# Optimization experiments

Measured on AMD Instinct MI355X. Metric: run time of the kernel, lower is better.

The kernel has to match this reference:

```python
import jax, jax.numpy as jnp
import numpy as np
import math

HIDDEN = 2048
NUM_HEADS = 16
NUM_KV_HEADS = 4
HEAD_DIM = 128
GROUPS = NUM_HEADS // NUM_KV_HEADS
BATCH = 1
SEQ = 4096
THETA = 10000.0


def _rope(x):
    # x: [B, h, S, D], interleaved-pair rotation as in the torch module
    seq = x.shape[2]
    freqs = 1.0 / (THETA ** (jnp.arange(0, HEAD_DIM, 2, dtype=jnp.float32) / HEAD_DIM))  # [D/2]
    angles = jnp.arange(seq, dtype=jnp.float32)[:, None] * freqs[None, :]  # [S, D/2]
    cos = jnp.cos(angles)[None, None]  # [1,1,S,D/2]
    sin = jnp.sin(angles)[None, None]
    x1 = x[..., 0::2]
    x2 = x[..., 1::2]
    # stack along new last axis then flatten -> interleaved layout
    rot = jnp.stack([x1 * cos - x2 * sin, x1 * sin + x2 * cos], axis=-1)
    return rot.reshape(x.shape)


def setup_inputs() -> dict:
    key = jax.random.key(0)
    kx, kq, kk, kv, ko = jax.random.split(key, 5)
    scale = 0.02
    x = jax.random.normal(kx, (BATCH, SEQ, HIDDEN), dtype=jnp.float32)
    Wq = jax.random.normal(kq, (NUM_HEADS * HEAD_DIM, HIDDEN), dtype=jnp.float32) * scale
    Wk = jax.random.normal(kk, (NUM_KV_HEADS * HEAD_DIM, HIDDEN), dtype=jnp.float32) * scale
    Wv = jax.random.normal(kv, (NUM_KV_HEADS * HEAD_DIM, HIDDEN), dtype=jnp.float32) * scale
    Wo = jax.random.normal(ko, (HIDDEN, NUM_HEADS * HEAD_DIM), dtype=jnp.float32) * scale
    return {"x": x, "Wq": Wq, "Wk": Wk, "Wv": Wv, "Wo": Wo}


def reference(x, Wq, Wk, Wv, Wo):
    B, S, _ = x.shape
    q = (x @ Wq.T).reshape(B, S, NUM_HEADS, HEAD_DIM).transpose(0, 2, 1, 3)      # [B,16,S,D]
    k = (x @ Wk.T).reshape(B, S, NUM_KV_HEADS, HEAD_DIM).transpose(0, 2, 1, 3)   # [B,4,S,D]
    v = (x @ Wv.T).reshape(B, S, NUM_KV_HEADS, HEAD_DIM).transpose(0, 2, 1, 3)
    q = _rope(q)
    k = _rope(k)
    # GQA: repeat_interleave KV heads across the group dim
    k = jnp.repeat(k, GROUPS, axis=1)  # [B,16,S,D]
    v = jnp.repeat(v, GROUPS, axis=1)
    scale = 1.0 / math.sqrt(HEAD_DIM)
    scores = jnp.einsum("bhqd,bhkd->bhqk", q, k) * scale  # [B,16,S,S]
    causal = jnp.triu(jnp.ones((S, S), dtype=bool), k=1)
    scores = jnp.where(causal[None, None], jnp.float32(-jnp.inf), scores)
    attn = jax.nn.softmax(scores, axis=-1)
    out = jnp.einsum("bhqk,bhkd->bhqd", attn, v)           # [B,16,S,D]
    out = out.transpose(0, 2, 1, 3).reshape(B, S, NUM_HEADS * HEAD_DIM)
    return out @ Wo.T
```

## Files before the change

### kernel.cpp

```cpp
#include <hip/hip_runtime.h>
#include <hip/hip_bf16.h>

typedef unsigned short u16;
typedef unsigned int u32;
typedef short short8 __attribute__((ext_vector_type(8)));
typedef unsigned short ushort4v __attribute__((ext_vector_type(4)));
typedef float f32x4 __attribute__((ext_vector_type(4)));
typedef float f32x16 __attribute__((ext_vector_type(16)));
typedef u32 u32x4 __attribute__((ext_vector_type(4)));

#define SEQN 4096
#define HID 2048
#define NH 16
#define NKV 4
#define HD 128
#define QDIM 2048
#define KVD 512
#define QKVS 3072

static __device__ __forceinline__ float bf2f(u16 u){
  unsigned x = ((unsigned)u) << 16; float f; __builtin_memcpy(&f, &x, 4); return f;
}
static __device__ __forceinline__ u16 f2bf(float f){
  unsigned x; __builtin_memcpy(&x, &f, 4);
  x += 0x7fffu + ((x >> 16) & 1u);
  return (u16)(x >> 16);
}
static __device__ __forceinline__ u32 pk2(float a, float b){
  return (u32)f2bf(a) | ((u32)f2bf(b) << 16);
}

__global__ __launch_bounds__(256) void cvt_kernel(const float* __restrict__ in, u16* __restrict__ out, int n4){
  int i = blockIdx.x * 256 + threadIdx.x;
  if (i >= n4) return;
  f32x4 v = ((const f32x4*)in)[i];
  ushort4v o;
  o.x = f2bf(v.x); o.y = f2bf(v.y); o.z = f2bf(v.z); o.w = f2bf(v.w);
  ((ushort4v*)out)[i] = o;
}

__global__ __launch_bounds__(256) void rope_kernel(u16* __restrict__ X, int stride, int nheads, int total){
  int idx = blockIdx.x * 256 + threadIdx.x;
  if (idx >= total) return;
  int i = idx & 63;
  int rest = idx >> 6;
  int h = rest % nheads;
  int s = rest / nheads;
  float freq = expf(-0.14391156831212788f * (float)i);
  float ang = (float)s * freq;
  float c = cosf(ang), sn = sinf(ang);
  u16* p = X + (size_t)s * stride + (size_t)h * HD + 2 * i;
  float x1 = bf2f(p[0]), x2 = bf2f(p[1]);
  p[0] = f2bf(x1 * c - x2 * sn);
  p[1] = f2bf(x1 * sn + x2 * c);
}

__global__ __launch_bounds__(256) void vtrans_kernel(const u16* __restrict__ V, int vstride, u16* __restrict__ VTg){
  __shared__ u16 T[64][72];
  const int s0 = blockIdx.x * 64;
  const int c0 = blockIdx.y * 64;
  const int tid = threadIdx.x;
  const int sl = tid & 63, ch = tid >> 6;
  const u16* src = V + (size_t)(s0 + sl) * vstride + c0 + ch * 16;
  *(short8*)&T[sl][ch * 16]     = *(const short8*)(src);
  *(short8*)&T[sl][ch * 16 + 8] = *(const short8*)(src + 8);
  __syncthreads();
#pragma unroll
  for (int it = 0; it < 16; it++){
    int c = it * 4 + ch;
    VTg[(size_t)(c0 + c) * SEQN + s0 + sl] = T[sl][c];
  }
}

static __device__ __forceinline__ void gload16(const void* g, void* l){
  __builtin_amdgcn_global_load_lds((const __attribute__((address_space(1))) void*)g,
                                   (__attribute__((address_space(3))) void*)l, 16, 0, 0);
}

template<int F32OUT>
__global__ __launch_bounds__(256) void gemm_kernel(const u16* __restrict__ A, const u16* __restrict__ B,
                                                   void* __restrict__ Cout, int M, int N, int Kd, int ldc){
  __shared__ alignas(16) u16 As[128 * 32];
  __shared__ alignas(16) u16 Bs[128 * 32];
  const int tid = threadIdx.x;
  const int w = tid >> 6, l = tid & 63;
  const int wr = w >> 1, wc = w & 1;
  const int lc = l & 15, lg = l >> 4;
  const int tm = blockIdx.x * 128, tn = blockIdx.y * 128;

  const int srow = w * 32 + (l >> 2);
  const int scol = (l & 3) * 8;
  const u16* Ag = A + (size_t)(tm + srow) * Kd + scol;
  const u16* Bg = B + (size_t)(tn + srow) * Kd + scol;
  u16* As0 = As + (w * 2) * 512;
  u16* Bs0 = Bs + (w * 2) * 512;

  f32x4 acc[4][4] = {};

  for (int k0 = 0; k0 < Kd; k0 += 32){
    gload16(Ag + k0,                    As0);
    gload16(Ag + k0 + (size_t)16 * Kd,  As0 + 512);
    gload16(Bg + k0,                    Bs0);
    gload16(Bg + k0 + (size_t)16 * Kd,  Bs0 + 512);
    __syncthreads();
    short8 a[4], b[4];
#pragma unroll
    for (int mi = 0; mi < 4; mi++) a[mi] = *(const short8*)&As[(wr*64 + mi*16 + lc) * 32 + lg*8];
#pragma unroll
    for (int ni = 0; ni < 4; ni++) b[ni] = *(const short8*)&Bs[(wc*64 + ni*16 + lc) * 32 + lg*8];
#pragma unroll
    for (int mi = 0; mi < 4; mi++)
#pragma unroll
      for (int ni = 0; ni < 4; ni++)
        acc[mi][ni] = __builtin_amdgcn_mfma_f32_16x16x32_bf16(a[mi], b[ni], acc[mi][ni], 0, 0, 0);
    __syncthreads();
  }

#pragma unroll
  for (int mi = 0; mi < 4; mi++)
#pragma unroll
    for (int ni = 0; ni < 4; ni++)
#pragma unroll
      for (int r = 0; r < 4; r++){
        int row = tm + wr*64 + mi*16 + lg*4 + r;
        int col = tn + wc*64 + ni*16 + lc;
        float v = acc[mi][ni][r];
        if (F32OUT) ((float*)Cout)[(size_t)row * ldc + col] = v;
        else        ((u16*)Cout)[(size_t)row * ldc + col] = f2bf(v);
      }
}

__global__ __launch_bounds__(256, 2) void attn_kernel(const u16* __restrict__ Qg, const u16* __restrict__ Kgb,
                                                      const u16* __restrict__ VTg, u16* __restrict__ Aout,
                                                      u16* __restrict__ PO, float* __restrict__ mP,
                                                      float* __restrict__ LP){
  __shared__ alignas(16) char pool[65536];

  const int pr  = blockIdx.x;
  const int h   = blockIdx.y;
  const int s   = blockIdx.z;
  const int kvh = h >> 2;
  const int tid = threadIdx.x;
  const int w = tid >> 6, l = tid & 63;
  const int q5 = l & 31;
  const int hi = l >> 5;
  const int hi4 = hi * 4;
  const float csc = 0.12751743f;

  const u16* Ksrc[4];
  const u16* Vsrc[4];
#pragma unroll
  for (int i = 0; i < 4; i++){
    int blk = w * 4 + i;
    int row = blk * 4 + (l >> 4);
    int cg  = (l & 15) ^ (row & 15);
    Ksrc[i] = Kgb + (size_t)row * QKVS + kvh * HD + cg * 8;
    int d   = blk * 8 + (l >> 3);
    int cv  = (l & 7) ^ (d & 7);
    Vsrc[i] = VTg + (size_t)(kvh * 128 + d) * SEQN + cv * 8;
  }

  auto issueTile = [&](int b, int kv0){
    char* Ksb = pool + b * 32768;
    char* VTb = Ksb + 16384;
#pragma unroll
    for (int i = 0; i < 4; i++)
      gload16(Ksrc[i] + (size_t)kv0 * QKVS, Ksb + (w * 4 + i) * 1024);
#pragma unroll
    for (int i = 0; i < 4; i++)
      gload16(Vsrc[i] + kv0, VTb + (w * 4 + i) * 1024);
  };

  const int qlo = pr, qhi = 31 - pr;
  int nseg, sq[2], st0[2], st1[2], smode[2];
  if (s == 0){
    nseg = 2;
    sq[0] = qlo; st0[0] = 0;           st1[0] = 2 * pr + 2;   smode[0] = 0;
    sq[1] = qhi; st0[1] = 0;           st1[1] = 31 - 2 * pr;  smode[1] = 1;
  } else {
    nseg = 1;
    sq[0] = qhi; st0[0] = 31 - 2 * pr; st1[0] = 64 - 2 * pr;  smode[0] = 2;
  }

  for (int sg = 0; sg < nseg; sg++){
    const int qt = sq[sg], t0 = st0[sg], t1 = st1[sg], mode = smode[sg];
    const int qbase = qt * 128 + w * 32;
    const int qa    = qbase + q5;

    short8 qf[8];
    {
      const u16* qp = Qg + (size_t)(qbase + q5) * QKVS + h * HD + hi * 8;
#pragma unroll
      for (int k0 = 0; k0 < 8; k0++) qf[k0] = *(const short8*)(qp + k0 * 16);
    }

    f32x16 Ov[4] = {};
    float Lrow = 0.f;
    float ms = -1e30f;

    auto computeTile = [&](int b, int kv0){
      if (kv0 > qbase + 31) return;
      char* Ksb = pool + b * 32768;
      char* VTb = Ksb + 16384;
      f32x16 Sv[2] = {};
#pragma unroll
      for (int k0 = 0; k0 < 8; k0++){
#pragma unroll
        for (int nb = 0; nb < 2; nb++){
          int kvr = nb * 32 + q5;
          short8 kf = *(const short8*)(Ksb + kvr * 256 + (((k0 * 2 + hi) ^ (kvr & 15)) << 4));
          Sv[nb] = __builtin_amdgcn_mfma_f32_32x32x16_bf16(kf, qf[k0], Sv[nb], 0, 0, 0);
        }
      }
      if (kv0 + 63 > qbase){
#pragma unroll
        for (int nb = 0; nb < 2; nb++)
#pragma unroll
          for (int r = 0; r < 16; r++){
            int kva = kv0 + nb * 32 + (r & 3) + 8 * (r >> 2) + hi4;
            if (kva > qa) Sv[nb][r] = -1e30f;
          }
      }
      float tm = -3e38f;
#pragma unroll
      for (int nb = 0; nb < 2; nb++)
#pragma unroll
        for (int r = 0; r < 16; r++) tm = fmaxf(tm, Sv[nb][r]);
      tm = fmaxf(tm, __shfl_xor(tm, 32));
      float tms = tm * csc;
      if (!__all(tms - ms <= 8.f)){
        float nms = fmaxf(ms, tms);
        float al = __builtin_amdgcn_exp2f(ms - nms);
        ms = nms;
        Lrow *= al;
#pragma unroll
        for (int nb = 0; nb < 4; nb++)
#pragma unroll
          for (int r = 0; r < 16; r++) Ov[nb][r] *= al;
      }
      float ts = 0.f;
#pragma unroll
      for (int nb = 0; nb < 2; nb++)
#pragma unroll
        for (int r = 0; r < 16; r++){
          float p = __builtin_amdgcn_exp2f(__builtin_fmaf(Sv[nb][r], csc, -ms));
          Sv[nb][r] = p;
          ts += p;
        }
      ts += __shfl_xor(ts, 32);
      Lrow += ts;
#pragma unroll
      for (int kc = 0; kc < 4; kc++){
        const int nb = kc >> 1, rb = (kc & 1) * 8;
        u32 Aw = pk2(Sv[nb][rb + 0], Sv[nb][rb + 1]);
        u32 Bw = pk2(Sv[nb][rb + 2], Sv[nb][rb + 3]);
        u32 Cw = pk2(Sv[nb][rb + 4], Sv[nb][rb + 5]);
        u32 Dw = pk2(Sv[nb][rb + 6], Sv[nb][rb + 7]);
        u32 sAw = __shfl_xor(Aw, 32);
        u32 sBw = __shfl_xor(Bw, 32);
        u32 sCw = __shfl_xor(Cw, 32);
        u32 sDw = __shfl_xor(Dw, 32);
        u32 w0 = hi ? sCw : Aw;
        u32 w1 = hi ? sDw : Bw;
        u32 w2 = hi ? Cw : sAw;
        u32 w3 = hi ? Dw : sBw;
        u32x4 pw4 = {w0, w1, w2, w3};
        short8 pf = *(short8*)&pw4;
#pragma unroll
        for (int nbd = 0; nbd < 4; nbd++){
          int drow = nbd * 32 + q5;
          short8 vf = *(const short8*)(VTb + drow * 128 + (((kc * 2 + hi) ^ (drow & 7)) << 4));
          Ov[nbd] = __builtin_amdgcn_mfma_f32_32x32x16_bf16(vf, pf, Ov[nbd], 0, 0, 0);
        }
      }
    };

    __syncthreads();
    issueTile(0, t0 * 64);
    __syncthreads();
    int cur = 0;
    for (int t = t0; t < t1; t++){
      if (t + 1 < t1) issueTile(cur ^ 1, (t + 1) * 64);
      computeTile(cur, t * 64);
      __syncthreads();
      cur ^= 1;
    }

    u16* Ew = (u16*)(pool + w * 8704);
    float rl = (mode == 0) ? (1.f / Lrow) : 1.f;
#pragma unroll
    for (int nbd = 0; nbd < 4; nbd++)
#pragma unroll
      for (int r = 0; r < 16; r += 2){
        int d = nbd * 32 + (r & 3) + 8 * (r >> 2) + hi4;
        u32 wpk = pk2(Ov[nbd][r] * rl, Ov[nbd][r + 1] * rl);
        *(u32*)((char*)Ew + q5 * 272 + d * 2) = wpk;
      }
    if (mode == 0){
#pragma unroll
      for (int pass = 0; pass < 8; pass++){
        int q2 = pass * 4 + (l >> 4);
        short8 ov = *(const short8*)((char*)Ew + q2 * 272 + (l & 15) * 16);
        *(short8*)(Aout + (size_t)(qbase + q2) * QDIM + h * HD + (l & 15) * 8) = ov;
      }
    } else {
      const int p = mode - 1;
      u16* dstb = PO + ((size_t)((p * 16 + pr) * NH + h) * 128) * 128;
#pragma unroll
      for (int pass = 0; pass < 8; pass++){
        int q2 = pass * 4 + (l >> 4);
        short8 ov = *(const short8*)((char*)Ew + q2 * 272 + (l & 15) * 16);
        *(short8*)(dstb + (size_t)(w * 32 + q2) * 128 + (l & 15) * 8) = ov;
      }
      if (hi == 0){
        int idx = ((p * 16 + pr) * NH + h) * 128 + w * 32 + q5;
        mP[idx] = ms;
        LP[idx] = Lrow;
      }
    }
  }
}

__global__ __launch_bounds__(256) void combine_kernel(const u16* __restrict__ PO, const float* __restrict__ mP,
                                                      const float* __restrict__ LP, u16* __restrict__ Aout){
  const int pr = blockIdx.x;
  const int h  = blockIdx.y;
  const int tid = threadIdx.x;
  const int r  = tid >> 1;
  const int dh = (tid & 1) * 64;
  const int qhi = 31 - pr;
  const int idx0 = ((0 * 16 + pr) * NH + h) * 128 + r;
  const int idx1 = ((1 * 16 + pr) * NH + h) * 128 + r;
  float m0 = mP[idx0], m1 = mP[idx1];
  float L0 = LP[idx0], L1 = LP[idx1];
  float M = fmaxf(m0, m1);
  float a0 = __builtin_amdgcn_exp2f(m0 - M);
  float a1 = __builtin_amdgcn_exp2f(m1 - M);
  float rl = 1.f / (L0 * a0 + L1 * a1);
  const u16* o0 = PO + (size_t)idx0 * 128 + dh;
  const u16* o1 = PO + (size_t)idx1 * 128 + dh;
  u16* dst = Aout + (size_t)(qhi * 128 + r) * QDIM + h * HD + dh;
#pragma unroll
  for (int ch = 0; ch < 8; ch++){
    short8 v0 = *(const short8*)(o0 + ch * 8);
    short8 v1 = *(const short8*)(o1 + ch * 8);
    short8 ov;
#pragma unroll
    for (int j = 0; j < 8; j++)
      ov[j] = (short)f2bf((bf2f((u16)v0[j]) * a0 + bf2f((u16)v1[j]) * a1) * rl);
    *(short8*)(dst + ch * 8) = ov;
  }
}

extern "C" void kernel_launch(void* const* d_in, const int* in_sizes, int n_in,
                              void* d_out, int out_size, void* d_ws, size_t ws_size,
                              hipStream_t stream){
  const float* x  = (const float*)d_in[0];
  const float* Wq = (const float*)d_in[1];
  const float* Wk = (const float*)d_in[2];
  const float* Wv = (const float*)d_in[3];
  const float* Wo = (const float*)d_in[4];

  char* p = (char*)d_ws;
  u16* xb    = (u16*)p; p += (size_t)SEQN * HID * 2;
  u16* Wqkvb = (u16*)p; p += (size_t)QKVS * HID * 2;
  u16* Wob   = (u16*)p; p += (size_t)HID * QDIM * 2;
  u16* QKVb  = (u16*)p; p += (size_t)SEQN * QKVS * 2;
  u16* Ab    = (u16*)p; p += (size_t)SEQN * QDIM * 2;
  u16* VTg   = (u16*)p; p += (size_t)SEQN * KVD * 2;
  u16* PO    = (u16*)p; p += (size_t)2 * 16 * NH * 128 * 128 * 2;
  float* mP  = (float*)p; p += (size_t)2 * 16 * NH * 128 * 4;
  float* LP  = (float*)p; p += (size_t)2 * 16 * NH * 128 * 4;

  cvt_kernel<<<(SEQN*HID/4 + 255)/256, 256, 0, stream>>>(x,  xb,  SEQN*HID/4);
  cvt_kernel<<<(QDIM*HID/4 + 255)/256, 256, 0, stream>>>(Wq, Wqkvb,                         QDIM*HID/4);
  cvt_kernel<<<(KVD*HID/4 + 255)/256, 256, 0, stream>>>(Wk, Wqkvb + (size_t)QDIM*HID,       KVD*HID/4);
  cvt_kernel<<<(KVD*HID/4 + 255)/256, 256, 0, stream>>>(Wv, Wqkvb + (size_t)(QDIM+KVD)*HID, KVD*HID/4);
  cvt_kernel<<<(HID*QDIM/4 + 255)/256, 256, 0, stream>>>(Wo, Wob, HID*QDIM/4);

  gemm_kernel<0><<<dim3(SEQN/128, QKVS/128), 256, 0, stream>>>(xb, Wqkvb, QKVb, SEQN, QKVS, HID, QKVS);

  rope_kernel<<<(SEQN*NH*64)/256,  256, 0, stream>>>(QKVb,        QKVS, NH,  SEQN*NH*64);
  rope_kernel<<<(SEQN*NKV*64)/256, 256, 0, stream>>>(QKVb + QDIM, QKVS, NKV, SEQN*NKV*64);

  vtrans_kernel<<<dim3(SEQN/64, KVD/64), 256, 0, stream>>>(QKVb + QDIM + KVD, QKVS, VTg);

  attn_kernel<<<dim3(16, NH, 2), 256, 0, stream>>>(QKVb, QKVb + QDIM, VTg, Ab, PO, mP, LP);
  combine_kernel<<<dim3(16, NH), 256, 0, stream>>>(PO, mP, LP, Ab);

  gemm_kernel<1><<<dim3(SEQN/128, HID/128), 256, 0, stream>>>(Ab, Wob, d_out, SEQN, HID, QDIM, HID);
}
```

Measured before the change: 267.0 us.

## Software-pipeline attention QK and PV phases, merge convert and rope launches

```diff
diff --git a/kernel.cpp b/kernel.cpp
--- a/kernel.cpp
+++ b/kernel.cpp
@@ -30,26 +30,41 @@
   return (u32)f2bf(a) | ((u32)f2bf(b) << 16);
 }
 
-__global__ __launch_bounds__(256) void cvt_kernel(const float* __restrict__ in, u16* __restrict__ out, int n4){
-  int i = blockIdx.x * 256 + threadIdx.x;
-  if (i >= n4) return;
-  f32x4 v = ((const f32x4*)in)[i];
+#define G1 (SEQN*HID/4)
+#define G2 (QDIM*HID/4)
+#define G3 (KVD*HID/4)
+#define G4 (KVD*HID/4)
+#define G5 (HID*QDIM/4)
+__global__ __launch_bounds__(256) void cvt5_kernel(const float* __restrict__ x,  const float* __restrict__ Wq,
+                                                   const float* __restrict__ Wk, const float* __restrict__ Wv,
+                                                   const float* __restrict__ Wo, u16* __restrict__ xb,
+                                                   u16* __restrict__ Wqkvb, u16* __restrict__ Wob){
+  int g = blockIdx.x * 256 + threadIdx.x;
+  const float* src; u16* dst; int off;
+  if (g < G1)                { src = x;  dst = xb;    off = g; }
+  else if (g < G1+G2)        { src = Wq; dst = Wqkvb; off = g - G1; }
+  else if (g < G1+G2+G3)     { src = Wk; dst = Wqkvb + (size_t)QDIM*HID/4*4;        off = g - (G1+G2); }
+  else if (g < G1+G2+G3+G4)  { src = Wv; dst = Wqkvb + (size_t)(QDIM+KVD)*HID/4*4;  off = g - (G1+G2+G3); }
+  else if (g < G1+G2+G3+G4+G5){ src = Wo; dst = Wob;  off = g - (G1+G2+G3+G4); }
+  else return;
+  f32x4 v = ((const f32x4*)src)[off];
   ushort4v o;
   o.x = f2bf(v.x); o.y = f2bf(v.y); o.z = f2bf(v.z); o.w = f2bf(v.w);
-  ((ushort4v*)out)[i] = o;
-}
-
-__global__ __launch_bounds__(256) void rope_kernel(u16* __restrict__ X, int stride, int nheads, int total){
+  ((ushort4v*)dst)[off] = o;
+}
+
+__global__ __launch_bounds__(256) void rope2_kernel(u16* __restrict__ QKVb){
   int idx = blockIdx.x * 256 + threadIdx.x;
-  if (idx >= total) return;
+  if (idx >= SEQN * (NH + NKV) * 64) return;
   int i = idx & 63;
   int rest = idx >> 6;
-  int h = rest % nheads;
-  int s = rest / nheads;
+  int h = rest % (NH + NKV);
+  int s = rest / (NH + NKV);
   float freq = expf(-0.14391156831212788f * (float)i);
   float ang = (float)s * freq;
   float c = cosf(ang), sn = sinf(ang);
-  u16* p = X + (size_t)s * stride + (size_t)h * HD + 2 * i;
+  int col = (h < NH) ? h * HD : QDIM + (h - NH) * HD;
+  u16* p = QKVb + (size_t)s * QKVS + col + 2 * i;
   float x1 = bf2f(p[0]), x2 = bf2f(p[1]);
   p[0] = f2bf(x1 * c - x2 * sn);
   p[1] = f2bf(x1 * sn + x2 * c);
@@ -134,7 +149,7 @@
                                                       const u16* __restrict__ VTg, u16* __restrict__ Aout,
                                                       u16* __restrict__ PO, float* __restrict__ mP,
                                                       float* __restrict__ LP){
-  __shared__ alignas(16) char pool[65536];
+  __shared__ alignas(16) char pool[81920];
 
   const int pr  = blockIdx.x;
   const int h   = blockIdx.y;
@@ -160,12 +175,14 @@
     Vsrc[i] = VTg + (size_t)(kvh * 128 + d) * SEQN + cv * 8;
   }
 
-  auto issueTile = [&](int b, int kv0){
-    char* Ksb = pool + b * 32768;
-    char* VTb = Ksb + 16384;
+  auto issueK = [&](int kb, int kv0){
+    char* Ksb = pool + kb * 16384;
 #pragma unroll
     for (int i = 0; i < 4; i++)
       gload16(Ksrc[i] + (size_t)kv0 * QKVS, Ksb + (w * 4 + i) * 1024);
+  };
+  auto issueV = [&](int vs, int kv0){
+    char* VTb = pool + 32768 + vs * 16384;
 #pragma unroll
     for (int i = 0; i < 4; i++)
       gload16(Vsrc[i] + kv0, VTb + (w * 4 + i) * 1024);
@@ -197,12 +214,12 @@
     f32x16 Ov[4] = {};
     float Lrow = 0.f;
     float ms = -1e30f;
-
-    auto computeTile = [&](int b, int kv0){
-      if (kv0 > qbase + 31) return;
-      char* Ksb = pool + b * 32768;
-      char* VTb = Ksb + 16384;
-      f32x16 Sv[2] = {};
+    f32x16 SvA[2], SvB[2];
+
+    auto qkPhase = [&](f32x16 (&Sv)[2], int kb){
+      char* Ksb = pool + kb * 16384;
+#pragma unroll
+      for (int r = 0; r < 16; r++){ Sv[0][r] = 0.f; Sv[1][r] = 0.f; }
 #pragma unroll
       for (int k0 = 0; k0 < 8; k0++){
 #pragma unroll
@@ -212,6 +229,10 @@
           Sv[nb] = __builtin_amdgcn_mfma_f32_32x32x16_bf16(kf, qf[k0], Sv[nb], 0, 0, 0);
         }
       }
+    };
+
+    auto finPhase = [&](f32x16 (&Sv)[2], int vs, int kv0){
+      char* VTb = pool + 32768 + vs * 16384;
       if (kv0 + 63 > qbase){
 #pragma unroll
         for (int nb = 0; nb < 2; nb++)
@@ -276,15 +297,33 @@
     };
 
     __syncthreads();
-    issueTile(0, t0 * 64);
+    issueK(0, t0 * 64); issueV(0, t0 * 64);
     __syncthreads();
-    int cur = 0;
-    for (int t = t0; t < t1; t++){
-      if (t + 1 < t1) issueTile(cur ^ 1, (t + 1) * 64);
-      computeTile(cur, t * 64);
-      __syncthreads();
-      cur ^= 1;
+
+    for (int t = t0; t < t1; t += 2){
+      {
+        int kb = (t - t0) & 1;
+        if (t + 1 < t1){ issueK(kb ^ 1, (t + 1) * 64); issueV((t + 1 - t0) % 3, (t + 1) * 64); }
+        if (t * 64 <= qbase + 31) qkPhase(SvA, kb);
+        if (t - 1 >= t0 && (t - 1) * 64 <= qbase + 31) finPhase(SvB, (t - 1 - t0) % 3, (t - 1) * 64);
+        __syncthreads();
+      }
+      if (t + 1 < t1){
+        int kb = (t + 1 - t0) & 1;
+        if (t + 2 < t1){ issueK(kb ^ 1, (t + 2) * 64); issueV((t + 2 - t0) % 3, (t + 2) * 64); }
+        if ((t + 1) * 64 <= qbase + 31) qkPhase(SvB, kb);
+        if (t * 64 <= qbase + 31) finPhase(SvA, (t - t0) % 3, t * 64);
+        __syncthreads();
+      }
     }
+    {
+      int tl = t1 - 1;
+      if (tl * 64 <= qbase + 31){
+        if ((tl - t0) & 1) finPhase(SvB, (tl - t0) % 3, tl * 64);
+        else               finPhase(SvA, (tl - t0) % 3, tl * 64);
+      }
+    }
+    __syncthreads();
 
     u16* Ew = (u16*)(pool + w * 8704);
     float rl = (mode == 0) ? (1.f / Lrow) : 1.f;
@@ -372,16 +411,12 @@
   float* mP  = (float*)p; p += (size_t)2 * 16 * NH * 128 * 4;
   float* LP  = (float*)p; p += (size_t)2 * 16 * NH * 128 * 4;
 
-  cvt_kernel<<<(SEQN*HID/4 + 255)/256, 256, 0, stream>>>(x,  xb,  SEQN*HID/4);
-  cvt_kernel<<<(QDIM*HID/4 + 255)/256, 256, 0, stream>>>(Wq, Wqkvb,                         QDIM*HID/4);
-  cvt_kernel<<<(KVD*HID/4 + 255)/256, 256, 0, stream>>>(Wk, Wqkvb + (size_t)QDIM*HID,       KVD*HID/4);
-  cvt_kernel<<<(KVD*HID/4 + 255)/256, 256, 0, stream>>>(Wv, Wqkvb + (size_t)(QDIM+KVD)*HID, KVD*HID/4);
-  cvt_kernel<<<(HID*QDIM/4 + 255)/256, 256, 0, stream>>>(Wo, Wob, HID*QDIM/4);
+  const int totg = G1 + G2 + G3 + G4 + G5;
+  cvt5_kernel<<<(totg + 255) / 256, 256, 0, stream>>>(x, Wq, Wk, Wv, Wo, xb, Wqkvb, Wob);
 
   gemm_kernel<0><<<dim3(SEQN/128, QKVS/128), 256, 0, stream>>>(xb, Wqkvb, QKVb, SEQN, QKVS, HID, QKVS);
 
-  rope_kernel<<<(SEQN*NH*64)/256,  256, 0, stream>>>(QKVb,        QKVS, NH,  SEQN*NH*64);
-  rope_kernel<<<(SEQN*NKV*64)/256, 256, 0, stream>>>(QKVb + QDIM, QKVS, NKV, SEQN*NKV*64);
+  rope2_kernel<<<(SEQN*(NH+NKV)*64 + 255) / 256, 256, 0, stream>>>(QKVb);
 
   vtrans_kernel<<<dim3(SEQN/64, KVD/64), 256, 0, stream>>>(QKVb + QDIM + KVD, QKVS, VTg);
 
```

Result: no change. 266.1 us (-0.3%).
